# Kernel tuning notes

Measured on AMD Instinct MI355X. Metric: run time of the kernel, lower is better.

The kernel has to match this reference:

```python
import jax, jax.numpy as jnp
import numpy as np

NUM_NODES = 120          # nodes per graph
B = 1024                 # graphs per batch
DEG = 16                 # avg degree
N = B * NUM_NODES        # total nodes
E = N * DEG              # total edges
C1 = NUM_NODES // 3      # conv1 out = 40
C2 = NUM_NODES // 2      # conv2 out = 60
OUT = 120


def _glorot(key, shape):
    fan = sum(shape) if len(shape) > 1 else shape[0] + 1
    return jax.random.normal(key, shape, jnp.float32) * jnp.sqrt(2.0 / fan)


def setup_inputs() -> dict:
    key = jax.random.key(0)
    ks = jax.random.split(key, 24)
    x = jax.random.normal(ks[0], (N, 3), jnp.float32)
    # block-structured edges: each edge stays inside its graph; no self-loops
    src_loc = jax.random.randint(ks[1], (B, NUM_NODES * DEG), 0, NUM_NODES)
    off = jax.random.randint(ks[2], (B, NUM_NODES * DEG), 1, NUM_NODES)
    dst_loc = (src_loc + off) % NUM_NODES
    base = (jnp.arange(B) * NUM_NODES)[:, None]
    edge_index = jnp.stack([(src_loc + base).reshape(-1), (dst_loc + base).reshape(-1)]).astype(jnp.int64)
    edge_attr = jax.random.uniform(ks[3], (E, 1), jnp.float32)
    mask = jax.random.uniform(ks[4], (B, OUT)) > 0.1
    p = {
        'W1': _glorot(ks[5], (3, C1)), 'att_src1': _glorot(ks[6], (C1,)),
        'att_dst1': _glorot(ks[7], (C1,)), 'We1': _glorot(ks[8], (1, C1)),
        'att_e1': _glorot(ks[9], (C1,)), 'b1': jnp.zeros((C1,), jnp.float32),
        'W2': _glorot(ks[10], (C1, C2)), 'att_src2': _glorot(ks[11], (C2,)),
        'att_dst2': _glorot(ks[12], (C2,)), 'We2': _glorot(ks[13], (1, C2)),
        'att_e2': _glorot(ks[14], (C2,)), 'b2': jnp.zeros((C2,), jnp.float32),
        'Wx1': _glorot(ks[15], (NUM_NODES * C2, NUM_NODES)), 'bx1': jnp.zeros((NUM_NODES,), jnp.float32),
        'Wx2': _glorot(ks[16], (NUM_NODES, OUT)), 'bx2': jnp.zeros((OUT,), jnp.float32),
    }
    return dict(x=x, edge_index=edge_index, edge_attr=edge_attr, mask=mask, **p)


def _segment_softmax(alpha, dst, n):
    m = jax.ops.segment_max(alpha, dst, num_segments=n)
    m = jnp.where(jnp.isfinite(m), m, 0.0)
    e = jnp.exp(alpha - m[dst])
    s = jax.ops.segment_sum(e, dst, num_segments=n)
    return e / (s[dst] + 1e-16)


def _gat_conv(x, edge_index, edge_attr, W, a_s, a_d, We, a_e, bias):
    n = x.shape[0]
    src, dst = edge_index[0], edge_index[1]
    # add self-loops; PyG fill_value='mean' -> self-loop edge_attr = mean over edges
    loop = jnp.arange(n, dtype=src.dtype)
    src = jnp.concatenate([src, loop])
    dst = jnp.concatenate([dst, loop])
    mean_attr = jnp.mean(edge_attr, axis=0, keepdims=True)            # [1, edge_dim]
    ea = jnp.concatenate([edge_attr, jnp.broadcast_to(mean_attr, (n, edge_attr.shape[1]))], 0)
    h = x @ W                                                          # [n, C]
    alpha_src = h @ a_s                                                # [n]
    alpha_dst = h @ a_d                                                # [n]
    alpha_edge = (ea @ We) @ a_e                                       # [E']
    alpha = jax.nn.leaky_relu(alpha_src[src] + alpha_dst[dst] + alpha_edge, 0.2)
    alpha = _segment_softmax(alpha, dst, n)                            # segment softmax over dst
    out = jax.ops.segment_sum(h[src] * alpha[:, None], dst, num_segments=n)
    return out + bias


def reference(x, edge_index, edge_attr, mask,
              W1, att_src1, att_dst1, We1, att_e1, b1,
              W2, att_src2, att_dst2, We2, att_e2, b2,
              Wx1, bx1, Wx2, bx2):
    out = _gat_conv(x, edge_index, edge_attr, W1, att_src1, att_dst1, We1, att_e1, b1)
    out = jax.nn.selu(out)
    out = _gat_conv(out, edge_index, edge_attr, W2, att_src2, att_dst2, We2, att_e2, b2)
    out = out.reshape(B, NUM_NODES * C2)          # stack(split) + flatten
    out = jax.nn.selu(out)
    out = jax.nn.selu(out @ Wx1 + bx1)
    out = out @ Wx2 + bx2
    return jnp.where(mask, out, -jnp.inf)
```

## Files before the change

kernel.cpp:

```cpp
#include <hip/hip_runtime.h>
#include <hip/hip_bf16.h>
#include <math.h>
#include <float.h>

#define NN   120
#define BGR  1024
#define NTOT (NN*BGR)
#define DEG  16
#define EPG  (NN*DEG)
#define ETOT (NTOT*DEG)
#define C1   40
#define C2   60
#define OUTD 120
#define KTOT 7200
#define KS   15
#define KCH  (KTOT/KS)
#define NP   128

#define SENTINEL (-1.0e30f)
#define FCLAMP   (3.3e38f)

#define OFF_A 256
#define OFF_B (OFF_A + NTOT*60*4)
#define OFF_C (OFF_B + NTOT*8)
#define OFF_D (OFF_C + NTOT*60*4)

typedef __attribute__((ext_vector_type(8))) short short8;
typedef __attribute__((ext_vector_type(4))) float f32x4;

__device__ __forceinline__ float seluf(float v){
    const float a = 1.6732632423543772f, sc = 1.0507009873554805f;
    return v > 0.f ? sc*v : sc*a*(__expf(v)-1.f);
}
__device__ __forceinline__ float lrelu(float v){ return v > 0.f ? v : 0.2f*v; }
__device__ __forceinline__ unsigned f2s(float f){ unsigned b=__float_as_uint(f); return (b&0x80000000u)? ~b : (b|0x80000000u); }
__device__ __forceinline__ float s2f(unsigned u){ return (u&0x80000000u)? __uint_as_float(u&0x7fffffffu) : __uint_as_float(~u); }
__device__ __forceinline__ float scrub(float v){
    return ((__float_as_uint(v)&0x7f800000u)==0x7f800000u) ? 0.f : v;
}
__device__ __forceinline__ unsigned short f2bf(float f){
    __hip_bfloat16 h = __float2bfloat16(f);
    return *reinterpret_cast<unsigned short*>(&h);
}

__global__ void k_detect(const int* __restrict__ ei, const unsigned char* __restrict__ maskb,
                         int* __restrict__ flags){
    __shared__ int c64, cm;
    int t = threadIdx.x;
    if (t==0){ c64=0; cm=0; }
    __syncthreads();
    if (t<64 && ei[2*t+1]!=0) atomicAdd(&c64,1);
    if (t<128 && maskb[t]!=0) atomicAdd(&cm,1);
    __syncthreads();
    if (t==0){
        flags[1] = (c64==0) ? 1 : 0;
        flags[2] = (cm>64) ? 1 : 0;
    }
}

__global__ __launch_bounds__(256) void k_mean(const float* __restrict__ ea, float* __restrict__ part){
    float acc = 0.f;
    for (int i = blockIdx.x*256 + threadIdx.x; i < ETOT; i += gridDim.x*256)
        acc += ea[i];
    for (int o=32;o>0;o>>=1) acc += __shfl_down(acc, o, 64);
    __shared__ float wsum[4];
    int lane = threadIdx.x & 63, w = threadIdx.x >> 6;
    if (lane==0) wsum[w]=acc;
    __syncthreads();
    if (threadIdx.x==0) part[blockIdx.x] = wsum[0]+wsum[1]+wsum[2]+wsum[3];
}
__global__ __launch_bounds__(256) void k_mean2(const float* __restrict__ part, float* __restrict__ wsf){
    int t = threadIdx.x;
    float acc = part[t] + part[t+256] + part[t+512] + part[t+768];
    for (int o=32;o>0;o>>=1) acc += __shfl_down(acc, o, 64);
    __shared__ float wsum[4];
    int lane = t & 63, w = t >> 6;
    if (lane==0) wsum[w]=acc;
    __syncthreads();
    if (t==0) wsf[0] = wsum[0]+wsum[1]+wsum[2]+wsum[3];
}

__global__ __launch_bounds__(256) void k_wt(const float* __restrict__ Wx1, unsigned short* __restrict__ Wt){
    __shared__ float tile[32][33];
    const int k0 = blockIdx.x*32, n0 = blockIdx.y*32;
    const int tx = threadIdx.x & 31, ty = threadIdx.x >> 5;
    #pragma unroll
    for (int rr=0; rr<4; ++rr){
        int r = ty*4+rr;
        int n = n0+tx;
        tile[r][tx] = (n<OUTD) ? Wx1[(size_t)(k0+r)*OUTD + n] : 0.f;
    }
    __syncthreads();
    #pragma unroll
    for (int rr=0; rr<4; ++rr){
        int r2 = ty*4+rr;
        Wt[(size_t)(n0+r2)*KTOT + k0 + tx] = f2bf(tile[tx][r2]);
    }
}

__global__ __launch_bounds__(256) void k_node2(const float* __restrict__ x1, const float* __restrict__ W2,
        const float* __restrict__ avs, const float* __restrict__ avd,
        float* __restrict__ h2, float* __restrict__ as2, float* __restrict__ ad2){
    int i = blockIdx.x*256 + threadIdx.x;
    float xr[C1];
    const float4* xp = (const float4*)(x1 + i*C1);
    #pragma unroll
    for (int q=0;q<C1/4;q++){ float4 v=xp[q]; xr[4*q]=v.x; xr[4*q+1]=v.y; xr[4*q+2]=v.z; xr[4*q+3]=v.w; }
    float hrow[C2];
    #pragma unroll
    for (int c=0;c<C2;c++) hrow[c]=0.f;
    #pragma unroll 4
    for (int k=0;k<C1;k++){
        float xv = xr[k];
        #pragma unroll
        for (int c=0;c<C2;c++) hrow[c] += xv*W2[k*C2+c];
    }
    float das=0.f, dad=0.f;
    #pragma unroll
    for (int c=0;c<C2;c++){ das += hrow[c]*avs[c]; dad += hrow[c]*avd[c]; }
    #pragma unroll
    for (int c=0;c<C2;c++) h2[i*C2+c] = hrow[c];
    as2[i]=das; ad2[i]=dad;
}

template<int NF4, bool OB16>
__device__ __forceinline__ void gather_row(
    int d, int jbase, int n, int off, float rs, float ws,
    const unsigned short* elist, const unsigned short* sd_s,
    const float* alpha_s, const float* h_s,
    const float* __restrict__ bias, char* __restrict__ xrow)
{
    const float4* hs4 = (const float4*)h_s;
    float4 acc[NF4];
    {
        int b = d*16, x7 = d&7;
        #pragma unroll
        for (int j=0;j<NF4;j++){
            float4 v = hs4[b + ((jbase+j)^x7)];
            acc[j].x=ws*v.x; acc[j].y=ws*v.y; acc[j].z=ws*v.z; acc[j].w=ws*v.w;
        }
    }
    int e = (n>0)? elist[off] : 0;
    for (int i=0;i<n;i++){
        int en = (i+1<n)? elist[off+i+1] : 0;
        float w = alpha_s[e];
        int s = sd_s[e]&255;
        int b = s*16, x7 = s&7;
        #pragma unroll
        for (int j=0;j<NF4;j++){
            float4 v = hs4[b + ((jbase+j)^x7)];
            acc[j].x += w*v.x; acc[j].y += w*v.y; acc[j].z += w*v.z; acc[j].w += w*v.w;
        }
        e = en;
    }
    #pragma unroll
    for (int j=0;j<NF4;j++){
        int ch = (jbase+j)*4;
        float o0 = seluf(rs*acc[j].x + bias[ch+0]);
        float o1 = seluf(rs*acc[j].y + bias[ch+1]);
        float o2 = seluf(rs*acc[j].z + bias[ch+2]);
        float o3 = seluf(rs*acc[j].w + bias[ch+3]);
        if constexpr (OB16){
            ushort4 o; o.x=f2bf(o0); o.y=f2bf(o1); o.z=f2bf(o2); o.w=f2bf(o3);
            ((ushort4*)xrow)[jbase+j] = o;
        } else {
            ((float4*)xrow)[jbase+j] = make_float4(o0,o1,o2,o3);
        }
    }
}

template<int C, int CLO, bool FUSE1, bool OB16>
__global__ __launch_bounds__(256) void k_conv(
    const int* __restrict__ ei, const float* __restrict__ ea,
    const float* __restrict__ hx,
    const float* __restrict__ asg, const float* __restrict__ adg,
    const float* __restrict__ Wn, const float* __restrict__ avs, const float* __restrict__ avd,
    const float* __restrict__ wsf, const float* __restrict__ We, const float* __restrict__ aev,
    const float* __restrict__ bias, char* __restrict__ xout)
{
    __shared__ float h_s[NN*64];
    __shared__ float alpha_s[EPG];
    __shared__ unsigned short sd_s[EPG];
    __shared__ unsigned short elist[EPG];
    __shared__ int cnt[128], cur[128], isum[128], offs[128];
    __shared__ unsigned m_s[128];
    __shared__ float asv[128], adv[128], sa_s[128], rs_s[128], wself_s[128];
    __shared__ float W1s[120];

    const int g=blockIdx.x, t=threadIdx.x;
    const int base=g*NN;
    const int is64 = ((const int*)wsf)[1];
    const float mean = wsf[0]*(1.0f/(float)ETOT);
    float cE=0.f;
    #pragma unroll
    for (int k=0;k<C;k++) cE += We[k]*aev[k];

    if (t<128){ cnt[t]=0; cur[t]=0; isum[t]=0; }

    if constexpr (FUSE1){
        for (int i=t;i<120;i+=256) W1s[i]=Wn[i];
        __syncthreads();
        if (t<2*NN){
            int n=t>>1, hf=t&1;
            const float* xr = hx + (size_t)(base+n)*3;
            float x0=xr[0],x1=xr[1],x2=xr[2];
            float hv[20]; float das=0.f,dad=0.f;
            #pragma unroll
            for (int cc=0;cc<20;cc++){
                int c=hf*20+cc;
                float hh = x0*W1s[c]+x1*W1s[40+c]+x2*W1s[80+c];
                hv[cc]=hh; das+=hh*avs[c]; dad+=hh*avd[c];
            }
            das += __shfl_xor(das,1,64);
            dad += __shfl_xor(dad,1,64);
            #pragma unroll
            for (int jj=0;jj<5;jj++){
                int j=hf*5+jj;
                ((float4*)h_s)[n*16+(j^(n&7))]=make_float4(hv[4*jj],hv[4*jj+1],hv[4*jj+2],hv[4*jj+3]);
            }
            if (hf==0){
                asv[n]=das; adv[n]=dad;
                float sa=lrelu(das+dad+cE*mean);
                sa_s[n]=sa; m_s[n]=f2s(sa);
            }
        }
    } else {
        const float4* hg=(const float4*)(hx+(size_t)base*C);
        for (int i=t;i<NN*(C/4);i+=256){
            int n=i/(C/4), j=i-n*(C/4);
            ((float4*)h_s)[n*16+(j^(n&7))]=hg[i];
        }
        for (int i=t;i<NN;i+=256){
            float a=asg[base+i], dd=adg[base+i];
            asv[i]=a; adv[i]=dd;
            float sa=lrelu(a+dd+cE*mean);
            sa_s[i]=sa; m_s[i]=f2s(sa);
        }
    }
    __syncthreads();

    const int gE = g*EPG;
    for (int e=t;e<EPG;e+=256){
        int s,d;
        if (is64){ s=ei[2*(gE+e)]; d=ei[2*(ETOT+gE+e)]; }
        else     { s=ei[gE+e];     d=ei[ETOT+gE+e];     }
        s-=base; d-=base; s&=127; d&=127;
        float a = lrelu(asv[s]+adv[d]+cE*ea[gE+e]);
        alpha_s[e]=a;
        sd_s[e]=(unsigned short)(s|(d<<8));
        atomicAdd(&cnt[d],1);
        atomicMax(&m_s[d], f2s(a));
    }
    __syncthreads();

    if (t<128) offs[t] = cnt[t];
    __syncthreads();
    #pragma unroll
    for (int s=1;s<128;s<<=1){
        int v=0;
        if (t<128 && t>=s) v = offs[t-s];
        __syncthreads();
        if (t<128 && t>=s) offs[t] += v;
        __syncthreads();
    }

    for (int e=t;e<EPG;e+=256){
        int d = sd_s[e]>>8;
        int pos = atomicAdd(&cur[d],1);
        elist[offs[d]-cnt[d]+pos] = (unsigned short)e;
    }
    __syncthreads();

    for (int e=t;e<EPG;e+=256){
        int d = sd_s[e]>>8;
        float w = __expf(alpha_s[e] - s2f(m_s[d]));
        alpha_s[e] = w;
        atomicAdd(&isum[d], (int)(w*16777216.0f));
    }
    __syncthreads();
    if (t<NN){
        float m = s2f(m_s[t]);
        float ws = __expf(sa_s[t]-m);
        float den = (float)isum[t]*5.9604645e-8f + ws;
        rs_s[t] = 1.0f/(den+1e-16f);
        wself_s[t] = ws;
    }
    __syncthreads();

    constexpr int NLO = CLO/4, NHI = (C-CLO)/4;
    constexpr int ROWB = C*(OB16?2:4);
    if (t < NN){
        int d=t, n=cnt[d], off=offs[d]-n;
        gather_row<NLO,OB16>(d, 0, n, off, rs_s[d], wself_s[d], elist, sd_s, alpha_s, h_s,
                             bias, xout + (size_t)(base+d)*ROWB);
    } else if (t < 2*NN){
        int d=t-NN, n=cnt[d], off=offs[d]-n;
        gather_row<NHI,OB16>(d, NLO, n, off, rs_s[d], wself_s[d], elist, sd_s, alpha_s, h_s,
                             bias, xout + (size_t)(base+d)*ROWB);
    }
}

__global__ __launch_bounds__(256) void k_fc1(const unsigned short* __restrict__ zb,
        const unsigned short* __restrict__ wt, float* __restrict__ y1p){
    const int t = threadIdx.x, w = t>>6, l = t&63;
    const int rt = w&1, chf = w>>1;
    const int m0 = blockIdx.x*32 + rt*16;
    const int c0 = chf*64;
    const int kb = blockIdx.y*KCH;
    const int lr = l&15, lk8 = (l>>4)*8;
    const unsigned short* za = zb + (size_t)(m0+lr)*KTOT + kb + lk8;
    const unsigned short* wa = wt + (size_t)(c0+lr)*KTOT + kb + lk8;
    f32x4 acc0={0,0,0,0}, acc1={0,0,0,0}, acc2={0,0,0,0}, acc3={0,0,0,0};
    #pragma unroll 5
    for (int ks=0; ks<KCH/32; ++ks){
        short8 a  = *(const short8*)(za + ks*32);
        short8 b0 = *(const short8*)(wa + 0*16*KTOT + ks*32);
        short8 b1 = *(const short8*)(wa + 1*16*KTOT + ks*32);
        short8 b2 = *(const short8*)(wa + 2*16*KTOT + ks*32);
        short8 b3 = *(const short8*)(wa + 3*16*KTOT + ks*32);
        acc0 = __builtin_amdgcn_mfma_f32_16x16x32_bf16(a, b0, acc0, 0,0,0);
        acc1 = __builtin_amdgcn_mfma_f32_16x16x32_bf16(a, b1, acc1, 0,0,0);
        acc2 = __builtin_amdgcn_mfma_f32_16x16x32_bf16(a, b2, acc2, 0,0,0);
        acc3 = __builtin_amdgcn_mfma_f32_16x16x32_bf16(a, b3, acc3, 0,0,0);
    }
    float* dst = y1p + (size_t)blockIdx.y*(BGR*NP) + (size_t)(m0 + (l>>4)*4)*NP + c0 + lr;
    #pragma unroll
    for (int r=0;r<4;r++){
        dst[r*NP + 0*16] = acc0[r];
        dst[r*NP + 1*16] = acc1[r];
        dst[r*NP + 2*16] = acc2[r];
        dst[r*NP + 3*16] = acc3[r];
    }
}

__global__ __launch_bounds__(128) void k_fc2(const float* __restrict__ y1p, const float* __restrict__ bx1,
        const float* __restrict__ Wx2, const float* __restrict__ bx2,
        const void* __restrict__ maskp, const int* __restrict__ flags, float* __restrict__ out){
    __shared__ float ys[OUTD];
    int g = blockIdx.x, t=threadIdx.x;
    for (int i=t;i<OUTD;i+=128){
        float a = bx1[i];
        #pragma unroll
        for (int s=0;s<KS;s++) a += y1p[s*(BGR*NP) + g*NP + i];
        ys[i] = seluf(a);
    }
    __syncthreads();
    if (t<OUTD){
        float a = bx2[t];
        for (int k=0;k<OUTD;k++) a += ys[k]*Wx2[k*OUTD+t];
        a = scrub(a);
        a = fminf(fmaxf(a, -FCLAMP), FCLAMP);
        bool mv;
        if (flags[2]) mv = ((const unsigned char*)maskp)[g*OUTD+t] != 0;
        else          mv = ((const int*)maskp)[g*OUTD+t] != 0;
        out[g*OUTD+t] = mv ? a : SENTINEL;
    }
}

extern "C" void kernel_launch(void* const* d_in, const int* in_sizes, int n_in,
                              void* d_out, int out_size, void* d_ws, size_t ws_size,
                              hipStream_t stream){
    const float* x    = (const float*)d_in[0];
    const int*   ei   = (const int*)d_in[1];
    const float* ea   = (const float*)d_in[2];
    const void*  mask = d_in[3];
    const float* W1   = (const float*)d_in[4];
    const float* as1v = (const float*)d_in[5];
    const float* ad1v = (const float*)d_in[6];
    const float* We1  = (const float*)d_in[7];
    const float* ae1  = (const float*)d_in[8];
    const float* b1   = (const float*)d_in[9];
    const float* W2   = (const float*)d_in[10];
    const float* as2v = (const float*)d_in[11];
    const float* ad2v = (const float*)d_in[12];
    const float* We2  = (const float*)d_in[13];
    const float* ae2  = (const float*)d_in[14];
    const float* b2   = (const float*)d_in[15];
    const float* Wx1  = (const float*)d_in[16];
    const float* bx1  = (const float*)d_in[17];
    const float* Wx2  = (const float*)d_in[18];
    const float* bx2  = (const float*)d_in[19];

    char* ws = (char*)d_ws;
    float* wsf  = (float*)ws;
    float* hbuf = (float*)(ws + OFF_A);
    float* asb  = (float*)(ws + OFF_B);
    float* adb  = asb + NTOT;
    float* xbuf = (float*)(ws + OFF_C);
    unsigned short* wt = (unsigned short*)(ws + OFF_D);
    float* y1p  = hbuf;
    float* outf = (float*)d_out;

    k_detect<<<1,128,0,stream>>>(ei, (const unsigned char*)mask, (int*)wsf);
    k_mean<<<1024,256,0,stream>>>(ea, asb);
    k_mean2<<<1,256,0,stream>>>(asb, wsf);
    {   dim3 gw(KTOT/32, NP/32);
        k_wt<<<gw,256,0,stream>>>(Wx1, wt); }
    k_conv<C1,20,true,false><<<BGR,256,0,stream>>>(ei, ea, x, nullptr, nullptr,
                                             W1, as1v, ad1v, wsf, We1, ae1, b1, (char*)xbuf);
    k_node2<<<NTOT/256,256,0,stream>>>(xbuf, W2, as2v, ad2v, hbuf, asb, adb);
    k_conv<C2,32,false,true><<<BGR,256,0,stream>>>(ei, ea, hbuf, asb, adb,
                                              nullptr, nullptr, nullptr, wsf, We2, ae2, b2, (char*)xbuf);
    dim3 g1(32, KS);
    k_fc1<<<g1,256,0,stream>>>((const unsigned short*)xbuf, wt, y1p);
    k_fc2<<<BGR,128,0,stream>>>(y1p, bx1, Wx2, bx2, mask, (const int*)wsf, outf);
}
```

Before: 265.7 us.

## Replace per-node edge gather with dense per-graph attention matrix MFMA

Each GAT conv block now builds a dense 128x128 attention matrix in shared memory, using integer fixed-point atomics for the softmax weights. The aggregation becomes a bf16 MFMA matmul against the transposed node features, replacing the CSR build (prefix scan, edge list) and the serial per-row gather loops. The conv2 node features are also stored as bf16 to halve global traffic. This adds 64KB+ of shared memory per block, which limits occupancy, and quantizes the attention weights and features to bf16 and fixed point, which risks accuracy.

```diff
diff --git a/kernel.cpp b/kernel.cpp
--- a/kernel.cpp
+++ b/kernel.cpp
@@ -27,6 +27,7 @@
 
 typedef __attribute__((ext_vector_type(8))) short short8;
 typedef __attribute__((ext_vector_type(4))) float f32x4;
+typedef __attribute__((ext_vector_type(4))) int   i32x4;
 
 __device__ __forceinline__ float seluf(float v){
     const float a = 1.6732632423543772f, sc = 1.0507009873554805f;
@@ -100,7 +101,7 @@
 
 __global__ __launch_bounds__(256) void k_node2(const float* __restrict__ x1, const float* __restrict__ W2,
         const float* __restrict__ avs, const float* __restrict__ avd,
-        float* __restrict__ h2, float* __restrict__ as2, float* __restrict__ ad2){
+        unsigned short* __restrict__ h2, float* __restrict__ as2, float* __restrict__ ad2){
     int i = blockIdx.x*256 + threadIdx.x;
     float xr[C1];
     const float4* xp = (const float4*)(x1 + i*C1);
@@ -119,72 +120,32 @@
     #pragma unroll
     for (int c=0;c<C2;c++){ das += hrow[c]*avs[c]; dad += hrow[c]*avd[c]; }
     #pragma unroll
-    for (int c=0;c<C2;c++) h2[i*C2+c] = hrow[c];
+    for (int c=0;c<C2;c+=2){
+        ushort2 u; u.x=f2bf(hrow[c]); u.y=f2bf(hrow[c+1]);
+        *(ushort2*)(h2 + (size_t)i*C2 + c) = u;
+    }
     as2[i]=das; ad2[i]=dad;
 }
 
-template<int NF4, bool OB16>
-__device__ __forceinline__ void gather_row(
-    int d, int jbase, int n, int off, float rs, float ws,
-    const unsigned short* elist, const unsigned short* sd_s,
-    const float* alpha_s, const float* h_s,
-    const float* __restrict__ bias, char* __restrict__ xrow)
-{
-    const float4* hs4 = (const float4*)h_s;
-    float4 acc[NF4];
-    {
-        int b = d*16, x7 = d&7;
-        #pragma unroll
-        for (int j=0;j<NF4;j++){
-            float4 v = hs4[b + ((jbase+j)^x7)];
-            acc[j].x=ws*v.x; acc[j].y=ws*v.y; acc[j].z=ws*v.z; acc[j].w=ws*v.w;
-        }
-    }
-    int e = (n>0)? elist[off] : 0;
-    for (int i=0;i<n;i++){
-        int en = (i+1<n)? elist[off+i+1] : 0;
-        float w = alpha_s[e];
-        int s = sd_s[e]&255;
-        int b = s*16, x7 = s&7;
-        #pragma unroll
-        for (int j=0;j<NF4;j++){
-            float4 v = hs4[b + ((jbase+j)^x7)];
-            acc[j].x += w*v.x; acc[j].y += w*v.y; acc[j].z += w*v.z; acc[j].w += w*v.w;
-        }
-        e = en;
-    }
-    #pragma unroll
-    for (int j=0;j<NF4;j++){
-        int ch = (jbase+j)*4;
-        float o0 = seluf(rs*acc[j].x + bias[ch+0]);
-        float o1 = seluf(rs*acc[j].y + bias[ch+1]);
-        float o2 = seluf(rs*acc[j].z + bias[ch+2]);
-        float o3 = seluf(rs*acc[j].w + bias[ch+3]);
-        if constexpr (OB16){
-            ushort4 o; o.x=f2bf(o0); o.y=f2bf(o1); o.z=f2bf(o2); o.w=f2bf(o3);
-            ((ushort4*)xrow)[jbase+j] = o;
-        } else {
-            ((float4*)xrow)[jbase+j] = make_float4(o0,o1,o2,o3);
-        }
-    }
-}
-
-template<int C, int CLO, bool FUSE1, bool OB16>
+template<int C, bool FUSE1, bool OB16>
 __global__ __launch_bounds__(256) void k_conv(
     const int* __restrict__ ei, const float* __restrict__ ea,
-    const float* __restrict__ hx,
+    const void* __restrict__ hx,
     const float* __restrict__ asg, const float* __restrict__ adg,
     const float* __restrict__ Wn, const float* __restrict__ avs, const float* __restrict__ avd,
     const float* __restrict__ wsf, const float* __restrict__ We, const float* __restrict__ aev,
-    const float* __restrict__ bias, char* __restrict__ xout)
+    const float* __restrict__ bias, void* __restrict__ xout)
 {
-    __shared__ float h_s[NN*64];
+    constexpr int NT  = (C+15)/16;
+    constexpr int OST = NT*16;
+    __shared__ int A_int[128*128];
+    __shared__ unsigned short ht[64*128];
     __shared__ float alpha_s[EPG];
     __shared__ unsigned short sd_s[EPG];
-    __shared__ unsigned short elist[EPG];
-    __shared__ int cnt[128], cur[128], isum[128], offs[128];
+    __shared__ __align__(16) char out_raw[OB16 ? NN*OST*2 : NN*OST*4];
     __shared__ unsigned m_s[128];
-    __shared__ float asv[128], adv[128], sa_s[128], rs_s[128], wself_s[128];
+    __shared__ float asv[128], adv[128], sa_s[128], rs_s[128];
+    __shared__ int isum[128];
     __shared__ float W1s[120];
 
     const int g=blockIdx.x, t=threadIdx.x;
@@ -195,29 +156,31 @@
     #pragma unroll
     for (int k=0;k<C;k++) cE += We[k]*aev[k];
 
-    if (t<128){ cnt[t]=0; cur[t]=0; isum[t]=0; }
+    for (int i=t;i<128*32;i+=256) ((i32x4*)A_int)[i] = (i32x4){0,0,0,0};
+    for (int i=t;i<64*16;i+=256)  ((short8*)ht)[i]   = (short8){0,0,0,0,0,0,0,0};
+    if (t<128){
+        isum[t]=0;
+        if (t>=NN){ asv[t]=0.f; adv[t]=0.f; sa_s[t]=0.f; m_s[t]=f2s(0.f); }
+    }
+    if constexpr (FUSE1){ for (int i=t;i<120;i+=256) W1s[i]=Wn[i]; }
+    __syncthreads();
 
     if constexpr (FUSE1){
-        for (int i=t;i<120;i+=256) W1s[i]=Wn[i];
-        __syncthreads();
+        const float* xg = (const float*)hx;
         if (t<2*NN){
             int n=t>>1, hf=t&1;
-            const float* xr = hx + (size_t)(base+n)*3;
+            const float* xr = xg + (size_t)(base+n)*3;
             float x0=xr[0],x1=xr[1],x2=xr[2];
-            float hv[20]; float das=0.f,dad=0.f;
+            float das=0.f,dad=0.f;
             #pragma unroll
             for (int cc=0;cc<20;cc++){
                 int c=hf*20+cc;
                 float hh = x0*W1s[c]+x1*W1s[40+c]+x2*W1s[80+c];
-                hv[cc]=hh; das+=hh*avs[c]; dad+=hh*avd[c];
+                das+=hh*avs[c]; dad+=hh*avd[c];
+                ht[c*128 + ((((n>>3))^(c&15))<<3) + (n&7)] = f2bf(hh);
             }
             das += __shfl_xor(das,1,64);
             dad += __shfl_xor(dad,1,64);
-            #pragma unroll
-            for (int jj=0;jj<5;jj++){
-                int j=hf*5+jj;
-                ((float4*)h_s)[n*16+(j^(n&7))]=make_float4(hv[4*jj],hv[4*jj+1],hv[4*jj+2],hv[4*jj+3]);
-            }
             if (hf==0){
                 asv[n]=das; adv[n]=dad;
                 float sa=lrelu(das+dad+cE*mean);
@@ -225,10 +188,10 @@
             }
         }
     } else {
-        const float4* hg=(const float4*)(hx+(size_t)base*C);
-        for (int i=t;i<NN*(C/4);i+=256){
-            int n=i/(C/4), j=i-n*(C/4);
-            ((float4*)h_s)[n*16+(j^(n&7))]=hg[i];
+        const unsigned short* hg = (const unsigned short*)hx + (size_t)base*C;
+        for (int i=t;i<NN*C;i+=256){
+            int n=i/C, c=i-n*C;
+            ht[c*128 + ((((n>>3))^(c&15))<<3) + (n&7)] = hg[i];
         }
         for (int i=t;i<NN;i+=256){
             float a=asg[base+i], dd=adg[base+i];
@@ -248,55 +211,85 @@
         float a = lrelu(asv[s]+adv[d]+cE*ea[gE+e]);
         alpha_s[e]=a;
         sd_s[e]=(unsigned short)(s|(d<<8));
-        atomicAdd(&cnt[d],1);
         atomicMax(&m_s[d], f2s(a));
     }
     __syncthreads();
 
-    if (t<128) offs[t] = cnt[t];
-    __syncthreads();
-    #pragma unroll
-    for (int s=1;s<128;s<<=1){
-        int v=0;
-        if (t<128 && t>=s) v = offs[t-s];
-        __syncthreads();
-        if (t<128 && t>=s) offs[t] += v;
-        __syncthreads();
-    }
-
     for (int e=t;e<EPG;e+=256){
-        int d = sd_s[e]>>8;
-        int pos = atomicAdd(&cur[d],1);
-        elist[offs[d]-cnt[d]+pos] = (unsigned short)e;
-    }
-    __syncthreads();
-
-    for (int e=t;e<EPG;e+=256){
-        int d = sd_s[e]>>8;
+        int sd=sd_s[e]; int s=sd&255, d=sd>>8;
         float w = __expf(alpha_s[e] - s2f(m_s[d]));
-        alpha_s[e] = w;
+        atomicAdd(&A_int[d*128 + (((s>>3)^(d&15))<<3) + (s&7)], (int)(w*8388608.0f));
         atomicAdd(&isum[d], (int)(w*16777216.0f));
     }
     __syncthreads();
-    if (t<NN){
+
+    if (t<128){
         float m = s2f(m_s[t]);
-        float ws = __expf(sa_s[t]-m);
-        float den = (float)isum[t]*5.9604645e-8f + ws;
+        float wself = __expf(sa_s[t]-m);
+        float den = (float)isum[t]*5.9604645e-8f + wself;
         rs_s[t] = 1.0f/(den+1e-16f);
-        wself_s[t] = ws;
-    }
-    __syncthreads();
-
-    constexpr int NLO = CLO/4, NHI = (C-CLO)/4;
-    constexpr int ROWB = C*(OB16?2:4);
-    if (t < NN){
-        int d=t, n=cnt[d], off=offs[d]-n;
-        gather_row<NLO,OB16>(d, 0, n, off, rs_s[d], wself_s[d], elist, sd_s, alpha_s, h_s,
-                             bias, xout + (size_t)(base+d)*ROWB);
-    } else if (t < 2*NN){
-        int d=t-NN, n=cnt[d], off=offs[d]-n;
-        gather_row<NHI,OB16>(d, NLO, n, off, rs_s[d], wself_s[d], elist, sd_s, alpha_s, h_s,
-                             bias, xout + (size_t)(base+d)*ROWB);
+        atomicAdd(&A_int[t*128 + (((t>>3)^(t&15))<<3) + (t&7)], (int)(wself*8388608.0f));
+    }
+    __syncthreads();
+
+    {
+        const int l = t&63, w = t>>6;
+        float* out_f = (float*)out_raw;
+        unsigned short* out_h = (unsigned short*)out_raw;
+        #pragma unroll
+        for (int mi=0; mi<2; ++mi){
+            const int mt = w*2 + mi;
+            const int m  = mt*16 + (l&15);
+            const float rsm = rs_s[m] * (1.1920929e-7f);
+            short8 afr[4];
+            #pragma unroll
+            for (int kc=0; kc<4; ++kc){
+                int k0 = kc*32 + (l>>4)*8;
+                const i32x4* p = (const i32x4*)(A_int + m*128 + (((k0>>3)^(l&15))<<3));
+                i32x4 i0 = p[0], i1 = p[1];
+                short8 r;
+                r[0]=(short)f2bf((float)i0[0]*rsm); r[1]=(short)f2bf((float)i0[1]*rsm);
+                r[2]=(short)f2bf((float)i0[2]*rsm); r[3]=(short)f2bf((float)i0[3]*rsm);
+                r[4]=(short)f2bf((float)i1[0]*rsm); r[5]=(short)f2bf((float)i1[1]*rsm);
+                r[6]=(short)f2bf((float)i1[2]*rsm); r[7]=(short)f2bf((float)i1[3]*rsm);
+                afr[kc]=r;
+            }
+            #pragma unroll
+            for (int nt=0; nt<NT; ++nt){
+                const int c = nt*16 + (l&15);
+                f32x4 acc = {0.f,0.f,0.f,0.f};
+                #pragma unroll
+                for (int kc=0; kc<4; ++kc){
+                    int k0 = kc*32 + (l>>4)*8;
+                    short8 b = *(const short8*)(ht + c*128 + (((k0>>3)^(c&15))<<3));
+                    acc = __builtin_amdgcn_mfma_f32_16x16x32_bf16(afr[kc], b, acc, 0,0,0);
+                }
+                if (c < C){
+                    const float bc = bias[c];
+                    const int mr0 = mt*16 + (l>>4)*4;
+                    #pragma unroll
+                    for (int r=0;r<4;r++){
+                        int mr = mr0 + r;
+                        if (mr < NN){
+                            float o = seluf(acc[r] + bc);
+                            if constexpr (OB16) out_h[mr*OST + c] = f2bf(o);
+                            else                out_f[mr*OST + c] = o;
+                        }
+                    }
+                }
+            }
+        }
+    }
+    __syncthreads();
+
+    if constexpr (OB16){
+        const unsigned short* out_h = (const unsigned short*)out_raw;
+        unsigned short* xo = (unsigned short*)xout + (size_t)base*C;
+        for (int i=t;i<NN*C;i+=256){ int n=i/C, c=i-n*C; xo[i] = out_h[n*OST+c]; }
+    } else {
+        const float* out_f = (const float*)out_raw;
+        float* xo = (float*)xout + (size_t)base*C;
+        for (int i=t;i<NN*C;i+=256){ int n=i/C, c=i-n*C; xo[i] = out_f[n*OST+c]; }
     }
 }
 
@@ -396,11 +389,11 @@
     k_mean2<<<1,256,0,stream>>>(asb, wsf);
     {   dim3 gw(KTOT/32, NP/32);
         k_wt<<<gw,256,0,stream>>>(Wx1, wt); }
-    k_conv<C1,20,true,false><<<BGR,256,0,stream>>>(ei, ea, x, nullptr, nullptr,
-                                             W1, as1v, ad1v, wsf, We1, ae1, b1, (char*)xbuf);
-    k_node2<<<NTOT/256,256,0,stream>>>(xbuf, W2, as2v, ad2v, hbuf, asb, adb);
-    k_conv<C2,32,false,true><<<BGR,256,0,stream>>>(ei, ea, hbuf, asb, adb,
-                                              nullptr, nullptr, nullptr, wsf, We2, ae2, b2, (char*)xbuf);
+    k_conv<C1,true,false><<<BGR,256,0,stream>>>(ei, ea, x, nullptr, nullptr,
+                                             W1, as1v, ad1v, wsf, We1, ae1, b1, xbuf);
+    k_node2<<<NTOT/256,256,0,stream>>>(xbuf, W2, as2v, ad2v, (unsigned short*)hbuf, asb, adb);
+    k_conv<C2,false,true><<<BGR,256,0,stream>>>(ei, ea, hbuf, asb, adb,
+                                              nullptr, nullptr, nullptr, wsf, We2, ae2, b2, xbuf);
     dim3 g1(32, KS);
     k_fc1<<<g1,256,0,stream>>>((const unsigned short*)xbuf, wt, y1p);
     k_fc2<<<BGR,128,0,stream>>>(y1p, bx1, Wx2, bx2, mask, (const int*)wsf, outf);
```

Measured after the change: 257.5 us. -3.1%, faster.
